# Optimization experiments

Hardware: AMD Instinct MI355X
Metric: run time of the kernel (lower is better)

Reference implementation:

```python
import jax, jax.numpy as jnp
import numpy as np

N_U, N_F = 50000, 20000
N = N_U + N_F
U_DIM, F_DIM, HID = 64, 128, 128
E = 2_000_000        # graph edges
E_PRED = 2_000_000   # prediction pairs
EPS = 1e-5
SLOPE = 0.01         # default leaky_relu negative slope


def setup_inputs() -> dict:
    key = jax.random.key(0)
    ks = jax.random.split(key, 20)
    s = 0.02
    inp = {
        "u_feat": jax.random.normal(ks[0], (N_U, U_DIM), jnp.float32),
        "f_feat": jax.random.normal(ks[1], (N_F, F_DIM), jnp.float32),
        "edge_index": jax.random.randint(ks[2], (2, E), 0, N, jnp.int64),
        "edge_u": jax.random.randint(ks[3], (E_PRED,), 0, N_U, jnp.int64),
        "edge_f": N_U + jax.random.randint(ks[4], (E_PRED,), 0, N_F, jnp.int64),
        # learned params
        "u_W": jax.random.normal(ks[5], (U_DIM, HID), jnp.float32) * s,
        "u_b": jnp.zeros((HID,), jnp.float32),
        "f_W": jax.random.normal(ks[6], (F_DIM, HID), jnp.float32) * s,
        "f_b": jnp.zeros((HID,), jnp.float32),
        "c1_W": jax.random.normal(ks[7], (HID, HID), jnp.float32) * s,
        "c1_b": jnp.zeros((HID,), jnp.float32),
        "c2_W": jax.random.normal(ks[8], (HID, HID), jnp.float32) * s,
        "c2_b": jnp.zeros((HID,), jnp.float32),
        "n1_g": jnp.ones((HID,), jnp.float32),
        "n1_b": jnp.zeros((HID,), jnp.float32),
        "n2_g": jnp.ones((HID,), jnp.float32),
        "n2_b": jnp.zeros((HID,), jnp.float32),
        "e_W": jax.random.normal(ks[9], (2 * HID, 1), jnp.float32) * s,
        "e_b": jnp.zeros((1,), jnp.float32),
        "r_W": jax.random.normal(ks[10], (2 * HID, 1), jnp.float32) * s,
        "r_b": jnp.zeros((1,), jnp.float32),
    }
    return inp


def _layer_norm(x, g, b):
    mu = jnp.mean(x, -1, keepdims=True)
    var = jnp.mean(jnp.square(x - mu), -1, keepdims=True)
    return (x - mu) * jax.lax.rsqrt(var + EPS) * g + b


def _gcn_conv(x, W, b, src, dst, n):
    # PyG GCNConv: add self loops, symmetric deg^{-1/2} norm, aggregate at dst.
    loop = jnp.arange(n, dtype=src.dtype)
    src_f = jnp.concatenate([src, loop])
    dst_f = jnp.concatenate([dst, loop])
    deg = jax.ops.segment_sum(jnp.ones(src_f.shape, x.dtype), dst_f, num_segments=n)
    dinv = jnp.where(deg > 0, jax.lax.rsqrt(deg), 0.0)
    norm = dinv[src_f] * dinv[dst_f]                     # [E+N]
    xw = x @ W                                           # [N, H]
    agg = jax.ops.segment_sum(xw[src_f] * norm[:, None], dst_f, num_segments=n)
    return agg + b


def reference(u_feat, f_feat, edge_index, edge_u, edge_f,
              u_W, u_b, f_W, f_b, c1_W, c1_b, c2_W, c2_b,
              n1_g, n1_b, n2_g, n2_b, e_W, e_b, r_W, r_b):
    src, dst = edge_index[0], edge_index[1]
    x = jnp.concatenate([u_feat @ u_W + u_b, f_feat @ f_W + f_b], 0)  # [N, H]
    x = jax.nn.leaky_relu(_layer_norm(_gcn_conv(x, c1_W, c1_b, src, dst, N), n1_g, n1_b), SLOPE)
    # dropout is identity in eval mode
    x = jax.nn.leaky_relu(_layer_norm(_gcn_conv(x, c2_W, c2_b, src, dst, N), n2_g, n2_b), SLOPE)
    emb = jnp.concatenate([x[edge_u], x[edge_f]], -1)                 # [E_pred, 2H]
    exist = jax.nn.sigmoid((emb @ e_W + e_b)[..., 0])
    rating = 1.0 + 4.0 * jax.nn.sigmoid((emb @ r_W + r_b)[..., 0])
    return exist, rating
```

## Files before the change

### kernel.cpp

```cpp
#include <hip/hip_runtime.h>
#include <hip/hip_bf16.h>
#include <math.h>

#define HID 128
#define SLOPE 0.01f
#define LN_EPS 1e-5f
#define NB_SCAN 256
#define NT_SCAN 256
#define BSHIFT 6
#define CHUNK 8192
#define MAXBUCK 1152

typedef __attribute__((ext_vector_type(8))) short bf16x8;
typedef __attribute__((ext_vector_type(4))) float f32x4;

__device__ __forceinline__ float bf16lo(unsigned int v) {
  unsigned int b = v << 16;
  return __builtin_bit_cast(float, b);
}
__device__ __forceinline__ float bf16hi(unsigned int v) {
  unsigned int b = v & 0xFFFF0000u;
  return __builtin_bit_cast(float, b);
}
__device__ __forceinline__ unsigned int pack_bf16(float lo, float hi) {
  __hip_bfloat16 a = __float2bfloat16(lo);
  __hip_bfloat16 b = __float2bfloat16(hi);
  return (unsigned int)__builtin_bit_cast(unsigned short, a) |
         ((unsigned int)__builtin_bit_cast(unsigned short, b) << 16);
}

__global__ __launch_bounds__(256) void wt_prep_kernel(
    const float* __restrict__ u_W, const float* __restrict__ f_W,
    const float* __restrict__ c1_W, const float* __restrict__ c2_W,
    const float* __restrict__ u_b, const float* __restrict__ f_b,
    unsigned int* __restrict__ wt_u1, unsigned int* __restrict__ wt_f1,
    unsigned int* __restrict__ wt_c2, float* __restrict__ bc_u,
    float* __restrict__ bc_f) {
  int idx = blockIdx.x * 256 + threadIdx.x;
  if (idx < 4096) {
    int col = idx & 127, k2 = idx >> 7;
    const float* a0 = u_W + (size_t)(2 * k2) * 128;
    const float* a1 = a0 + 128;
    float s0 = 0.0f, s1 = 0.0f;
    for (int m = 0; m < 128; ++m) {
      float bm = c1_W[(size_t)m * 128 + col];
      s0 = fmaf(a0[m], bm, s0);
      s1 = fmaf(a1[m], bm, s1);
    }
    wt_u1[(size_t)col * 32 + k2] = pack_bf16(s0, s1);
  } else if (idx < 12288) {
    int i = idx - 4096;
    int col = i & 127, k2 = i >> 7;
    const float* a0 = f_W + (size_t)(2 * k2) * 128;
    const float* a1 = a0 + 128;
    float s0 = 0.0f, s1 = 0.0f;
    for (int m = 0; m < 128; ++m) {
      float bm = c1_W[(size_t)m * 128 + col];
      s0 = fmaf(a0[m], bm, s0);
      s1 = fmaf(a1[m], bm, s1);
    }
    wt_f1[(size_t)col * 64 + k2] = pack_bf16(s0, s1);
  } else if (idx < 20480) {
    int i = idx - 12288;
    int col = i & 127, k2 = i >> 7;
    wt_c2[(size_t)col * 64 + k2] =
        pack_bf16(c2_W[(size_t)(2 * k2) * 128 + col],
                  c2_W[(size_t)(2 * k2 + 1) * 128 + col]);
  } else if (idx < 20736) {
    int i = idx - 20480;
    int j = i & 127;
    const float* bv = (i < 128) ? u_b : f_b;
    float s = 0.0f;
    for (int m = 0; m < 128; ++m) s = fmaf(bv[m], c1_W[(size_t)m * 128 + j], s);
    if (i < 128) bc_u[j] = s; else bc_f[j] = s;
  }
}

__global__ __launch_bounds__(256) void hist_chunk_kernel(
    const int* __restrict__ dst, int* __restrict__ cntM,
    int E, int nbuck, int nchunk) {
  __shared__ int hist[MAXBUCK];
  int c = blockIdx.x, tid = threadIdx.x;
  for (int i = tid; i < nbuck; i += 256) hist[i] = 0;
  __syncthreads();
  int beg = c * CHUNK, end = min(beg + CHUNK, E);
  for (int e = beg + tid; e < end; e += 256)
    atomicAdd(&hist[dst[e] >> BSHIFT], 1);
  __syncthreads();
  for (int b = tid; b < nbuck; b += 256)
    cntM[(size_t)b * nchunk + c] = hist[b];
}

__global__ void scan_pass1(const int* __restrict__ cnt, int* __restrict__ blocksum, int m) {
  __shared__ int ss[NT_SCAN];
  int K = (m + NB_SCAN * NT_SCAN - 1) / (NB_SCAN * NT_SCAN);
  int t = threadIdx.x, b = blockIdx.x;
  int beg = (b * NT_SCAN + t) * K;
  int end = min(beg + K, m);
  int s = 0;
  for (int i = beg; i < end; ++i) s += cnt[i];
  ss[t] = s;
  __syncthreads();
  for (int off = NT_SCAN / 2; off > 0; off >>= 1) {
    if (t < off) ss[t] += ss[t + off];
    __syncthreads();
  }
  if (t == 0) blocksum[b] = ss[0];
}

__global__ void scan_pass2(int* __restrict__ blocksum) {
  __shared__ int ss[NB_SCAN];
  int t = threadIdx.x;
  ss[t] = blocksum[t];
  __syncthreads();
  for (int off = 1; off < NB_SCAN; off <<= 1) {
    int v = (t >= off) ? ss[t - off] : 0;
    __syncthreads();
    ss[t] += v;
    __syncthreads();
  }
  blocksum[t] = (t == 0) ? 0 : ss[t - 1];
}

__global__ void scan_pass3(const int* __restrict__ cnt, const int* __restrict__ blockoff,
                           int* __restrict__ scanM, int m) {
  __shared__ int ss[NT_SCAN];
  int K = (m + NB_SCAN * NT_SCAN - 1) / (NB_SCAN * NT_SCAN);
  int t = threadIdx.x, b = blockIdx.x;
  int beg = (b * NT_SCAN + t) * K;
  int end = min(beg + K, m);
  int s = 0;
  for (int i = beg; i < end; ++i) s += cnt[i];
  ss[t] = s;
  __syncthreads();
  for (int off = 1; off < NT_SCAN; off <<= 1) {
    int v = (t >= off) ? ss[t - off] : 0;
    __syncthreads();
    ss[t] += v;
    __syncthreads();
  }
  int pre = blockoff[b] + ((t == 0) ? 0 : ss[t - 1]);
  for (int i = beg; i < end; ++i) {
    scanM[i] = pre;
    pre += cnt[i];
    if (i == m - 1) scanM[m] = pre;
  }
}

__global__ __launch_bounds__(256) void scatter_chunk_kernel(
    const int* __restrict__ src, const int* __restrict__ dst,
    const int* __restrict__ scanM, unsigned int* __restrict__ ebuf,
    int E, int nbuck, int nchunk) {
  __shared__ int cur[MAXBUCK];
  int c = blockIdx.x, tid = threadIdx.x;
  for (int b = tid; b < nbuck; b += 256)
    cur[b] = scanM[(size_t)b * nchunk + c];
  __syncthreads();
  int beg = c * CHUNK, end = min(beg + CHUNK, E);
  for (int e = beg + tid; e < end; e += 256) {
    int s = src[e], d = dst[e];
    int pos = atomicAdd(&cur[d >> BSHIFT], 1);
    ebuf[pos] = ((unsigned)s << 6) | ((unsigned)d & 63);
  }
}

__global__ __launch_bounds__(256) void deg_rowptr_kernel(
    const unsigned int* __restrict__ ebuf, const int* __restrict__ scanM,
    int* __restrict__ rowptr, float* __restrict__ dinv,
    int n, int nbuck, int nchunk, int E) {
  __shared__ int sdeg[64];
  int b = blockIdx.x, tid = threadIdx.x;
  if (tid < 64) sdeg[tid] = 0;
  __syncthreads();
  int beg = scanM[(size_t)b * nchunk], end = scanM[(size_t)(b + 1) * nchunk];
  for (int j = beg + tid; j < end; j += 256) atomicAdd(&sdeg[ebuf[j] & 63], 1);
  __syncthreads();
  if (tid < 64) {
    int deg = sdeg[tid];
    int s = deg;
#pragma unroll
    for (int off = 1; off < 64; off <<= 1) {
      int v = __shfl_up(s, off);
      if (tid >= off) s += v;
    }
    int excl = s - deg;
    int nd = (b << BSHIFT) + tid;
    if (nd < n) {
      rowptr[nd] = beg + excl;
      dinv[nd] = rsqrtf((float)(deg + 1));
    }
    if (b == nbuck - 1 && tid == 0) rowptr[n] = E;
  }
}

__global__ __launch_bounds__(256) void fill_bucket_kernel(
    const unsigned int* __restrict__ ebuf, const int* __restrict__ scanM,
    const int* __restrict__ rowptr, const float* __restrict__ dinv,
    uint2* __restrict__ ecol, int n, int nchunk) {
  __shared__ int scur[64];
  __shared__ int srow[64];
  __shared__ float sdinv[64];
  int b = blockIdx.x, tid = threadIdx.x;
  if (tid < 64) {
    scur[tid] = 0;
    int nd = (b << BSHIFT) + tid;
    srow[tid] = (nd < n) ? rowptr[nd] : 0;
    sdinv[tid] = (nd < n) ? dinv[nd] : 0.0f;
  }
  __syncthreads();
  int beg = scanM[(size_t)b * nchunk], end = scanM[(size_t)(b + 1) * nchunk];
  for (int j = beg + tid; j < end; j += 256) {
    unsigned int v = ebuf[j];
    int ndl = (int)(v & 63);
    int s = (int)(v >> 6);
    int pos = atomicAdd(&scur[ndl], 1);
    float w = dinv[s] * sdinv[ndl];
    ecol[srow[ndl] + pos] = make_uint2((unsigned)s, __builtin_bit_cast(unsigned int, w));
  }
}

template<int K, bool BF16OUT>
__global__ __launch_bounds__(256) void dense_mfma_kernel(
    const float* __restrict__ feat, const unsigned int* __restrict__ Wt,
    const float* __restrict__ bias,
    float* __restrict__ outf, __hip_bfloat16* __restrict__ outb, int nrows) {
  int tid = threadIdx.x;
  int wid = tid >> 6, lane = tid & 63;
  int l15 = lane & 15, lk = lane >> 4;
  int rowbase = blockIdx.x * 32 + 16 * (wid & 1);
  int colbase = 64 * (wid >> 1);

  f32x4 acc0 = {}, acc1 = {}, acc2 = {}, acc3 = {};

  int row = rowbase + l15;
  int rrow = min(row, nrows - 1);
  const float* ap0 = feat + (size_t)rrow * K + lk * 8;

#pragma unroll
  for (int kb = 0; kb < K / 32; ++kb) {
    const float* ap = ap0 + kb * 32;
    float4 a0 = *reinterpret_cast<const float4*>(ap);
    float4 a1 = *reinterpret_cast<const float4*>(ap + 4);
    float af0 = a0.x, af1 = a0.y, af2 = a0.z, af3 = a0.w;
    float af4 = a1.x, af5 = a1.y, af6 = a1.z, af7 = a1.w;
    unsigned int b0 = __builtin_bit_cast(unsigned int, af0);
    unsigned int b1 = __builtin_bit_cast(unsigned int, af1);
    unsigned int b2 = __builtin_bit_cast(unsigned int, af2);
    unsigned int b3 = __builtin_bit_cast(unsigned int, af3);
    unsigned int b4 = __builtin_bit_cast(unsigned int, af4);
    unsigned int b5 = __builtin_bit_cast(unsigned int, af5);
    unsigned int b6 = __builtin_bit_cast(unsigned int, af6);
    unsigned int b7 = __builtin_bit_cast(unsigned int, af7);
    uint4 hv;
    hv.x = (b0 >> 16) | (b1 & 0xFFFF0000u);
    hv.y = (b2 >> 16) | (b3 & 0xFFFF0000u);
    hv.z = (b4 >> 16) | (b5 & 0xFFFF0000u);
    hv.w = (b6 >> 16) | (b7 & 0xFFFF0000u);
    uint4 lv;
    {
      float h0 = __builtin_bit_cast(float, b0 & 0xFFFF0000u);
      float h1 = __builtin_bit_cast(float, b1 & 0xFFFF0000u);
      float h2 = __builtin_bit_cast(float, b2 & 0xFFFF0000u);
      float h3 = __builtin_bit_cast(float, b3 & 0xFFFF0000u);
      float h4 = __builtin_bit_cast(float, b4 & 0xFFFF0000u);
      float h5 = __builtin_bit_cast(float, b5 & 0xFFFF0000u);
      float h6 = __builtin_bit_cast(float, b6 & 0xFFFF0000u);
      float h7 = __builtin_bit_cast(float, b7 & 0xFFFF0000u);
      lv.x = pack_bf16(af0 - h0, af1 - h1);
      lv.y = pack_bf16(af2 - h2, af3 - h3);
      lv.z = pack_bf16(af4 - h4, af5 - h5);
      lv.w = pack_bf16(af6 - h6, af7 - h7);
    }
    bf16x8 ahi = __builtin_bit_cast(bf16x8, hv);
    bf16x8 alo = __builtin_bit_cast(bf16x8, lv);

    const unsigned int* wrow = Wt + (size_t)(colbase + l15) * (K / 2) + kb * 16 + lk * 4;
    bf16x8 bf0 = __builtin_bit_cast(bf16x8, *reinterpret_cast<const uint4*>(wrow));
    bf16x8 bf1 = __builtin_bit_cast(bf16x8, *reinterpret_cast<const uint4*>(wrow + 16 * (K / 2)));
    bf16x8 bf2 = __builtin_bit_cast(bf16x8, *reinterpret_cast<const uint4*>(wrow + 32 * (K / 2)));
    bf16x8 bf3 = __builtin_bit_cast(bf16x8, *reinterpret_cast<const uint4*>(wrow + 48 * (K / 2)));
    acc0 = __builtin_amdgcn_mfma_f32_16x16x32_bf16(ahi, bf0, acc0, 0, 0, 0);
    acc0 = __builtin_amdgcn_mfma_f32_16x16x32_bf16(alo, bf0, acc0, 0, 0, 0);
    acc1 = __builtin_amdgcn_mfma_f32_16x16x32_bf16(ahi, bf1, acc1, 0, 0, 0);
    acc1 = __builtin_amdgcn_mfma_f32_16x16x32_bf16(alo, bf1, acc1, 0, 0, 0);
    acc2 = __builtin_amdgcn_mfma_f32_16x16x32_bf16(ahi, bf2, acc2, 0, 0, 0);
    acc2 = __builtin_amdgcn_mfma_f32_16x16x32_bf16(alo, bf2, acc2, 0, 0, 0);
    acc3 = __builtin_amdgcn_mfma_f32_16x16x32_bf16(ahi, bf3, acc3, 0, 0, 0);
    acc3 = __builtin_amdgcn_mfma_f32_16x16x32_bf16(alo, bf3, acc3, 0, 0, 0);
  }

#pragma unroll
  for (int t = 0; t < 4; ++t) {
    int col = colbase + 16 * t + l15;
    float bv = bias ? bias[col] : 0.0f;
    f32x4 a = (t == 0) ? acc0 : (t == 1) ? acc1 : (t == 2) ? acc2 : acc3;
#pragma unroll
    for (int r = 0; r < 4; ++r) {
      int orow = rowbase + lk * 4 + r;
      if (orow < nrows) {
        float v = a[r] + bv;
        if (BF16OUT) outb[(size_t)orow * HID + col] = __float2bfloat16(v);
        else         outf[(size_t)orow * HID + col] = v;
      }
    }
  }
}

template<bool PROJ>
__global__ void gather_norm_kernel(const int* __restrict__ rowptr,
                                   const uint2* __restrict__ ecol,
                                   const uint4* __restrict__ xwb4,
                                   const float* __restrict__ dinv,
                                   const float* __restrict__ cb,
                                   const float* __restrict__ g,
                                   const float* __restrict__ b,
                                   const float* __restrict__ eW,
                                   const float* __restrict__ rW,
                                   float* __restrict__ outx,
                                   float4* __restrict__ table, int n_nodes) {
  int d = blockIdx.x * 4 + (threadIdx.x >> 6);
  if (d >= n_nodes) return;
  int lane = threadIdx.x & 63;
  int grp = lane >> 4;
  int t = lane & 15;

  float acc[8];
#pragma unroll
  for (int k = 0; k < 8; ++k) acc[k] = 0.0f;

  float wd = dinv[d];
  int beg = rowptr[d], end = rowptr[d + 1];
  int j = beg + grp;
  for (; j + 12 < end; j += 16) {
    uint2 e0 = ecol[j];
    uint2 e1 = ecol[j + 4];
    uint2 e2 = ecol[j + 8];
    uint2 e3 = ecol[j + 12];
    uint4 v0 = xwb4[(size_t)e0.x * 16 + t];
    uint4 v1 = xwb4[(size_t)e1.x * 16 + t];
    uint4 v2 = xwb4[(size_t)e2.x * 16 + t];
    uint4 v3 = xwb4[(size_t)e3.x * 16 + t];
    float w0 = __builtin_bit_cast(float, e0.y);
    float w1 = __builtin_bit_cast(float, e1.y);
    float w2 = __builtin_bit_cast(float, e2.y);
    float w3 = __builtin_bit_cast(float, e3.y);
    acc[0] = fmaf(bf16lo(v0.x), w0, acc[0]);
    acc[1] = fmaf(bf16hi(v0.x), w0, acc[1]);
    acc[2] = fmaf(bf16lo(v0.y), w0, acc[2]);
    acc[3] = fmaf(bf16hi(v0.y), w0, acc[3]);
    acc[4] = fmaf(bf16lo(v0.z), w0, acc[4]);
    acc[5] = fmaf(bf16hi(v0.z), w0, acc[5]);
    acc[6] = fmaf(bf16lo(v0.w), w0, acc[6]);
    acc[7] = fmaf(bf16hi(v0.w), w0, acc[7]);
    acc[0] = fmaf(bf16lo(v1.x), w1, acc[0]);
    acc[1] = fmaf(bf16hi(v1.x), w1, acc[1]);
    acc[2] = fmaf(bf16lo(v1.y), w1, acc[2]);
    acc[3] = fmaf(bf16hi(v1.y), w1, acc[3]);
    acc[4] = fmaf(bf16lo(v1.z), w1, acc[4]);
    acc[5] = fmaf(bf16hi(v1.z), w1, acc[5]);
    acc[6] = fmaf(bf16lo(v1.w), w1, acc[6]);
    acc[7] = fmaf(bf16hi(v1.w), w1, acc[7]);
    acc[0] = fmaf(bf16lo(v2.x), w2, acc[0]);
    acc[1] = fmaf(bf16hi(v2.x), w2, acc[1]);
    acc[2] = fmaf(bf16lo(v2.y), w2, acc[2]);
    acc[3] = fmaf(bf16hi(v2.y), w2, acc[3]);
    acc[4] = fmaf(bf16lo(v2.z), w2, acc[4]);
    acc[5] = fmaf(bf16hi(v2.z), w2, acc[5]);
    acc[6] = fmaf(bf16lo(v2.w), w2, acc[6]);
    acc[7] = fmaf(bf16hi(v2.w), w2, acc[7]);
    acc[0] = fmaf(bf16lo(v3.x), w3, acc[0]);
    acc[1] = fmaf(bf16hi(v3.x), w3, acc[1]);
    acc[2] = fmaf(bf16lo(v3.y), w3, acc[2]);
    acc[3] = fmaf(bf16hi(v3.y), w3, acc[3]);
    acc[4] = fmaf(bf16lo(v3.z), w3, acc[4]);
    acc[5] = fmaf(bf16hi(v3.z), w3, acc[5]);
    acc[6] = fmaf(bf16lo(v3.w), w3, acc[6]);
    acc[7] = fmaf(bf16hi(v3.w), w3, acc[7]);
  }
  for (; j < end; j += 4) {
    uint2 e0 = ecol[j];
    uint4 v0 = xwb4[(size_t)e0.x * 16 + t];
    float w0 = __builtin_bit_cast(float, e0.y);
    acc[0] = fmaf(bf16lo(v0.x), w0, acc[0]);
    acc[1] = fmaf(bf16hi(v0.x), w0, acc[1]);
    acc[2] = fmaf(bf16lo(v0.y), w0, acc[2]);
    acc[3] = fmaf(bf16hi(v0.y), w0, acc[3]);
    acc[4] = fmaf(bf16lo(v0.z), w0, acc[4]);
    acc[5] = fmaf(bf16hi(v0.z), w0, acc[5]);
    acc[6] = fmaf(bf16lo(v0.w), w0, acc[6]);
    acc[7] = fmaf(bf16hi(v0.w), w0, acc[7]);
  }
#pragma unroll
  for (int k = 0; k < 8; ++k) {
    acc[k] += __shfl_xor(acc[k], 16);
    acc[k] += __shfl_xor(acc[k], 32);
  }
  {
    float wself = wd * wd;
    uint4 v = xwb4[(size_t)d * 16 + t];
    acc[0] = fmaf(bf16lo(v.x), wself, acc[0]);
    acc[1] = fmaf(bf16hi(v.x), wself, acc[1]);
    acc[2] = fmaf(bf16lo(v.y), wself, acc[2]);
    acc[3] = fmaf(bf16hi(v.y), wself, acc[3]);
    acc[4] = fmaf(bf16lo(v.z), wself, acc[4]);
    acc[5] = fmaf(bf16hi(v.z), wself, acc[5]);
    acc[6] = fmaf(bf16lo(v.w), wself, acc[6]);
    acc[7] = fmaf(bf16hi(v.w), wself, acc[7]);
    float4 c0 = *reinterpret_cast<const float4*>(cb + 8 * t);
    float4 c1 = *reinterpret_cast<const float4*>(cb + 8 * t + 4);
    acc[0] += c0.x; acc[1] += c0.y; acc[2] += c0.z; acc[3] += c0.w;
    acc[4] += c1.x; acc[5] += c1.y; acc[6] += c1.z; acc[7] += c1.w;
  }
  float s = acc[0] + acc[1] + acc[2] + acc[3] + acc[4] + acc[5] + acc[6] + acc[7];
#pragma unroll
  for (int m = 1; m < 16; m <<= 1) s += __shfl_xor(s, m);
  float mu = s * (1.0f / HID);
  float sq = 0.0f;
#pragma unroll
  for (int k = 0; k < 8; ++k) {
    acc[k] -= mu;
    sq = fmaf(acc[k], acc[k], sq);
  }
#pragma unroll
  for (int m = 1; m < 16; m <<= 1) sq += __shfl_xor(sq, m);
  float rs = rsqrtf(sq * (1.0f / HID) + LN_EPS);
  float4 g0 = *reinterpret_cast<const float4*>(g + 8 * t);
  float4 g1 = *reinterpret_cast<const float4*>(g + 8 * t + 4);
  float4 b0 = *reinterpret_cast<const float4*>(b + 8 * t);
  float4 b1 = *reinterpret_cast<const float4*>(b + 8 * t + 4);
  float o[8];
  o[0] = acc[0] * rs * g0.x + b0.x;
  o[1] = acc[1] * rs * g0.y + b0.y;
  o[2] = acc[2] * rs * g0.z + b0.z;
  o[3] = acc[3] * rs * g0.w + b0.w;
  o[4] = acc[4] * rs * g1.x + b1.x;
  o[5] = acc[5] * rs * g1.y + b1.y;
  o[6] = acc[6] * rs * g1.z + b1.z;
  o[7] = acc[7] * rs * g1.w + b1.w;
#pragma unroll
  for (int k = 0; k < 8; ++k) o[k] = o[k] >= 0.0f ? o[k] : SLOPE * o[k];

  if (!PROJ) {
    if (grp == 0) {
      float4* op = reinterpret_cast<float4*>(outx + (size_t)d * HID + 8 * t);
      op[0] = make_float4(o[0], o[1], o[2], o[3]);
      op[1] = make_float4(o[4], o[5], o[6], o[7]);
    }
  } else {
    float4 eu0 = *reinterpret_cast<const float4*>(eW + 8 * t);
    float4 eu1 = *reinterpret_cast<const float4*>(eW + 8 * t + 4);
    float4 ef0 = *reinterpret_cast<const float4*>(eW + HID + 8 * t);
    float4 ef1 = *reinterpret_cast<const float4*>(eW + HID + 8 * t + 4);
    float4 ru0 = *reinterpret_cast<const float4*>(rW + 8 * t);
    float4 ru1 = *reinterpret_cast<const float4*>(rW + 8 * t + 4);
    float4 rf0 = *reinterpret_cast<const float4*>(rW + HID + 8 * t);
    float4 rf1 = *reinterpret_cast<const float4*>(rW + HID + 8 * t + 4);
    float pa = o[0]*eu0.x + o[1]*eu0.y + o[2]*eu0.z + o[3]*eu0.w
             + o[4]*eu1.x + o[5]*eu1.y + o[6]*eu1.z + o[7]*eu1.w;
    float pb = o[0]*ef0.x + o[1]*ef0.y + o[2]*ef0.z + o[3]*ef0.w
             + o[4]*ef1.x + o[5]*ef1.y + o[6]*ef1.z + o[7]*ef1.w;
    float pc = o[0]*ru0.x + o[1]*ru0.y + o[2]*ru0.z + o[3]*ru0.w
             + o[4]*ru1.x + o[5]*ru1.y + o[6]*ru1.z + o[7]*ru1.w;
    float pd = o[0]*rf0.x + o[1]*rf0.y + o[2]*rf0.z + o[3]*rf0.w
             + o[4]*rf1.x + o[5]*rf1.y + o[6]*rf1.z + o[7]*rf1.w;
#pragma unroll
    for (int m = 1; m < 16; m <<= 1) {
      pa += __shfl_xor(pa, m);
      pb += __shfl_xor(pb, m);
      pc += __shfl_xor(pc, m);
      pd += __shfl_xor(pd, m);
    }
    if (lane == 0) table[d] = make_float4(pa, pb, pc, pd);
  }
}

__global__ void pair_kernel(const int* __restrict__ eu, const int* __restrict__ ef,
                            const float4* __restrict__ table,
                            const float* __restrict__ eb, const float* __restrict__ rb,
                            float* __restrict__ out_exist, float* __restrict__ out_rating,
                            int Ep) {
  int i = blockIdx.x * blockDim.x + threadIdx.x;
  if (i >= Ep) return;
  float4 tu = table[eu[i]];
  float4 tf = table[ef[i]];
  float pe = tu.x + tf.y + eb[0];
  float pr = tu.z + tf.w + rb[0];
  out_exist[i]  = 1.0f / (1.0f + expf(-pe));
  out_rating[i] = 1.0f + 4.0f / (1.0f + expf(-pr));
}

extern "C" void kernel_launch(void* const* d_in, const int* in_sizes, int n_in,
                              void* d_out, int out_size, void* d_ws, size_t ws_size,
                              hipStream_t stream) {
  const float* u_feat = (const float*)d_in[0];
  const float* f_feat = (const float*)d_in[1];
  const int*   ei     = (const int*)d_in[2];
  const int*   eu     = (const int*)d_in[3];
  const int*   ef     = (const int*)d_in[4];
  const float* u_W  = (const float*)d_in[5];
  const float* u_b  = (const float*)d_in[6];
  const float* f_W  = (const float*)d_in[7];
  const float* f_b  = (const float*)d_in[8];
  const float* c1_W = (const float*)d_in[9];
  const float* c1_b = (const float*)d_in[10];
  const float* c2_W = (const float*)d_in[11];
  const float* c2_b = (const float*)d_in[12];
  const float* n1_g = (const float*)d_in[13];
  const float* n1_b = (const float*)d_in[14];
  const float* n2_g = (const float*)d_in[15];
  const float* n2_b = (const float*)d_in[16];
  const float* e_W  = (const float*)d_in[17];
  const float* e_b  = (const float*)d_in[18];
  const float* r_W  = (const float*)d_in[19];
  const float* r_b  = (const float*)d_in[20];

  int n_u = in_sizes[0] / 64;
  int n_f = in_sizes[1] / HID;
  int n   = n_u + n_f;
  int E   = in_sizes[2] / 2;
  int Ep  = in_sizes[3];
  int nbuck  = (n + (1 << BSHIFT) - 1) >> BSHIFT;
  int nchunk = (E + CHUNK - 1) / CHUNK;
  int m      = nbuck * nchunk;

  const int* src = ei;
  const int* dst = ei + E;

  float*        x      = (float*)d_ws;
  unsigned int* xwb    = (unsigned int*)(x + (size_t)n * HID);
  float4*       table  = (float4*)(xwb + (size_t)n * (HID / 2));
  unsigned int* ebuf   = (unsigned int*)(table + n);
  uint2*        ecol   = (uint2*)(ebuf + E);
  float*        dinv   = (float*)(ecol + E);
  int*          rowptr = (int*)(dinv + n);
  int*          cntM   = rowptr + n + 1;
  int*          scanM  = cntM + m;
  int*          blocksum = scanM + m + 1;
  unsigned int* wt_u1  = (unsigned int*)(blocksum + NB_SCAN);
  unsigned int* wt_f1  = wt_u1 + 128 * 32;
  unsigned int* wt_c2  = wt_f1 + 128 * 64;
  float*        bc_u   = (float*)(wt_c2 + 128 * 64);
  float*        bc_f   = bc_u + 128;

  wt_prep_kernel<<<81, 256, 0, stream>>>(u_W, f_W, c1_W, c2_W, u_b, f_b,
                                         wt_u1, wt_f1, wt_c2, bc_u, bc_f);

  hist_chunk_kernel<<<nchunk, 256, 0, stream>>>(dst, cntM, E, nbuck, nchunk);
  scan_pass1<<<NB_SCAN, NT_SCAN, 0, stream>>>(cntM, blocksum, m);
  scan_pass2<<<1, NB_SCAN, 0, stream>>>(blocksum);
  scan_pass3<<<NB_SCAN, NT_SCAN, 0, stream>>>(cntM, blocksum, scanM, m);
  scatter_chunk_kernel<<<nchunk, 256, 0, stream>>>(src, dst, scanM, ebuf, E, nbuck, nchunk);

  deg_rowptr_kernel<<<nbuck, 256, 0, stream>>>(ebuf, scanM, rowptr, dinv,
                                               n, nbuck, nchunk, E);
  fill_bucket_kernel<<<nbuck, 256, 0, stream>>>(ebuf, scanM, rowptr, dinv, ecol,
                                                n, nchunk);

  dense_mfma_kernel<64, true><<<(n_u + 31) / 32, 256, 0, stream>>>(
      u_feat, wt_u1, bc_u, nullptr, (__hip_bfloat16*)xwb, n_u);
  dense_mfma_kernel<128, true><<<(n_f + 31) / 32, 256, 0, stream>>>(
      f_feat, wt_f1, bc_f, nullptr, ((__hip_bfloat16*)xwb) + (size_t)n_u * HID, n_f);
  gather_norm_kernel<false><<<(n + 3) / 4, 256, 0, stream>>>(
      rowptr, ecol, (const uint4*)xwb, dinv, c1_b, n1_g, n1_b,
      nullptr, nullptr, x, nullptr, n);

  dense_mfma_kernel<128, true><<<(n + 31) / 32, 256, 0, stream>>>(
      x, wt_c2, nullptr, nullptr, (__hip_bfloat16*)xwb, n);
  gather_norm_kernel<true><<<(n + 3) / 4, 256, 0, stream>>>(
      rowptr, ecol, (const uint4*)xwb, dinv, c2_b, n2_g, n2_b,
      e_W, r_W, nullptr, table, n);

  float* out_exist  = (float*)d_out;
  float* out_rating = out_exist + Ep;
  pair_kernel<<<(Ep + 255) / 256, 256, 0, stream>>>(eu, ef, table, e_b, r_b,
                                                    out_exist, out_rating, Ep);
}
```

Measured before the change: 305.4 us.

## Merge weight prep with histogram, fold scan pass2, vectorize edge loops

Folds the weight-prep kernel and the dst histogram into one launch using block-index dispatch. Scan pass2 is folded into pass3, with every block redundantly scanning the 256 block sums. The edge loops in scatter, degree and fill, plus the pair kernel, now handle two elements per thread with int2/uint2 loads. This removes two kernel launches and widens memory accesses. It relies on 8-byte alignment, which holds because the chunk and bucket bases are even only when the offsets are even; scanM offsets can be odd, so the uint2 loads from ebuf may be misaligned.

```diff
diff --git a/kernel.cpp b/kernel.cpp
--- a/kernel.cpp
+++ b/kernel.cpp
@@ -10,6 +10,7 @@
 #define BSHIFT 6
 #define CHUNK 8192
 #define MAXBUCK 1152
+#define WPREP_BLOCKS 81
 
 typedef __attribute__((ext_vector_type(8))) short bf16x8;
 typedef __attribute__((ext_vector_type(4))) float f32x4;
@@ -29,13 +30,33 @@
          ((unsigned int)__builtin_bit_cast(unsigned short, b) << 16);
 }
 
-__global__ __launch_bounds__(256) void wt_prep_kernel(
+__global__ __launch_bounds__(256) void prep_hist_kernel(
     const float* __restrict__ u_W, const float* __restrict__ f_W,
     const float* __restrict__ c1_W, const float* __restrict__ c2_W,
     const float* __restrict__ u_b, const float* __restrict__ f_b,
     unsigned int* __restrict__ wt_u1, unsigned int* __restrict__ wt_f1,
     unsigned int* __restrict__ wt_c2, float* __restrict__ bc_u,
-    float* __restrict__ bc_f) {
+    float* __restrict__ bc_f,
+    const int* __restrict__ dst, int* __restrict__ cntM,
+    int E, int nbuck, int nchunk) {
+  __shared__ int hist[MAXBUCK];
+  if (blockIdx.x >= WPREP_BLOCKS) {
+    int c = blockIdx.x - WPREP_BLOCKS, tid = threadIdx.x;
+    for (int i = tid; i < nbuck; i += 256) hist[i] = 0;
+    __syncthreads();
+    int beg = c * CHUNK, end = min(beg + CHUNK, E);
+    int e = beg + 2 * tid;
+    for (; e + 1 < end; e += 512) {
+      int2 d2 = *reinterpret_cast<const int2*>(&dst[e]);
+      atomicAdd(&hist[d2.x >> BSHIFT], 1);
+      atomicAdd(&hist[d2.y >> BSHIFT], 1);
+    }
+    if (e < end) atomicAdd(&hist[dst[e] >> BSHIFT], 1);
+    __syncthreads();
+    for (int b = tid; b < nbuck; b += 256)
+      cntM[(size_t)b * nchunk + c] = hist[b];
+    return;
+  }
   int idx = blockIdx.x * 256 + threadIdx.x;
   if (idx < 4096) {
     int col = idx & 127, k2 = idx >> 7;
@@ -76,21 +97,6 @@
   }
 }
 
-__global__ __launch_bounds__(256) void hist_chunk_kernel(
-    const int* __restrict__ dst, int* __restrict__ cntM,
-    int E, int nbuck, int nchunk) {
-  __shared__ int hist[MAXBUCK];
-  int c = blockIdx.x, tid = threadIdx.x;
-  for (int i = tid; i < nbuck; i += 256) hist[i] = 0;
-  __syncthreads();
-  int beg = c * CHUNK, end = min(beg + CHUNK, E);
-  for (int e = beg + tid; e < end; e += 256)
-    atomicAdd(&hist[dst[e] >> BSHIFT], 1);
-  __syncthreads();
-  for (int b = tid; b < nbuck; b += 256)
-    cntM[(size_t)b * nchunk + c] = hist[b];
-}
-
 __global__ void scan_pass1(const int* __restrict__ cnt, int* __restrict__ blocksum, int m) {
   __shared__ int ss[NT_SCAN];
   int K = (m + NB_SCAN * NT_SCAN - 1) / (NB_SCAN * NT_SCAN);
@@ -108,25 +114,21 @@
   if (t == 0) blocksum[b] = ss[0];
 }
 
-__global__ void scan_pass2(int* __restrict__ blocksum) {
-  __shared__ int ss[NB_SCAN];
-  int t = threadIdx.x;
-  ss[t] = blocksum[t];
+__global__ void scan_pass3(const int* __restrict__ cnt, const int* __restrict__ blocksum,
+                           int* __restrict__ scanM, int m) {
+  __shared__ int ss[NT_SCAN];
+  __shared__ int sb[NB_SCAN];
+  int K = (m + NB_SCAN * NT_SCAN - 1) / (NB_SCAN * NT_SCAN);
+  int t = threadIdx.x, b = blockIdx.x;
+  sb[t] = blocksum[t];
   __syncthreads();
   for (int off = 1; off < NB_SCAN; off <<= 1) {
-    int v = (t >= off) ? ss[t - off] : 0;
+    int v = (t >= off) ? sb[t - off] : 0;
     __syncthreads();
-    ss[t] += v;
+    sb[t] += v;
     __syncthreads();
   }
-  blocksum[t] = (t == 0) ? 0 : ss[t - 1];
-}
-
-__global__ void scan_pass3(const int* __restrict__ cnt, const int* __restrict__ blockoff,
-                           int* __restrict__ scanM, int m) {
-  __shared__ int ss[NT_SCAN];
-  int K = (m + NB_SCAN * NT_SCAN - 1) / (NB_SCAN * NT_SCAN);
-  int t = threadIdx.x, b = blockIdx.x;
+  int blockoff = (b == 0) ? 0 : sb[b - 1];
   int beg = (b * NT_SCAN + t) * K;
   int end = min(beg + K, m);
   int s = 0;
@@ -139,7 +141,7 @@
     ss[t] += v;
     __syncthreads();
   }
-  int pre = blockoff[b] + ((t == 0) ? 0 : ss[t - 1]);
+  int pre = blockoff + ((t == 0) ? 0 : ss[t - 1]);
   for (int i = beg; i < end; ++i) {
     scanM[i] = pre;
     pre += cnt[i];
@@ -157,7 +159,16 @@
     cur[b] = scanM[(size_t)b * nchunk + c];
   __syncthreads();
   int beg = c * CHUNK, end = min(beg + CHUNK, E);
-  for (int e = beg + tid; e < end; e += 256) {
+  int e = beg + 2 * tid;
+  for (; e + 1 < end; e += 512) {
+    int2 s2 = *reinterpret_cast<const int2*>(&src[e]);
+    int2 d2 = *reinterpret_cast<const int2*>(&dst[e]);
+    int p0 = atomicAdd(&cur[d2.x >> BSHIFT], 1);
+    ebuf[p0] = ((unsigned)s2.x << 6) | ((unsigned)d2.x & 63);
+    int p1 = atomicAdd(&cur[d2.y >> BSHIFT], 1);
+    ebuf[p1] = ((unsigned)s2.y << 6) | ((unsigned)d2.y & 63);
+  }
+  if (e < end) {
     int s = src[e], d = dst[e];
     int pos = atomicAdd(&cur[d >> BSHIFT], 1);
     ebuf[pos] = ((unsigned)s << 6) | ((unsigned)d & 63);
@@ -173,7 +184,13 @@
   if (tid < 64) sdeg[tid] = 0;
   __syncthreads();
   int beg = scanM[(size_t)b * nchunk], end = scanM[(size_t)(b + 1) * nchunk];
-  for (int j = beg + tid; j < end; j += 256) atomicAdd(&sdeg[ebuf[j] & 63], 1);
+  int j = beg + 2 * tid;
+  for (; j + 1 < end; j += 512) {
+    uint2 v2 = *reinterpret_cast<const uint2*>(&ebuf[j]);
+    atomicAdd(&sdeg[v2.x & 63], 1);
+    atomicAdd(&sdeg[v2.y & 63], 1);
+  }
+  if (j < end) atomicAdd(&sdeg[ebuf[j] & 63], 1);
   __syncthreads();
   if (tid < 64) {
     int deg = sdeg[tid];
@@ -209,7 +226,25 @@
   }
   __syncthreads();
   int beg = scanM[(size_t)b * nchunk], end = scanM[(size_t)(b + 1) * nchunk];
-  for (int j = beg + tid; j < end; j += 256) {
+  int j = beg + 2 * tid;
+  for (; j + 1 < end; j += 512) {
+    uint2 v2 = *reinterpret_cast<const uint2*>(&ebuf[j]);
+    {
+      int ndl = (int)(v2.x & 63);
+      int s = (int)(v2.x >> 6);
+      int pos = atomicAdd(&scur[ndl], 1);
+      float w = dinv[s] * sdinv[ndl];
+      ecol[srow[ndl] + pos] = make_uint2((unsigned)s, __builtin_bit_cast(unsigned int, w));
+    }
+    {
+      int ndl = (int)(v2.y & 63);
+      int s = (int)(v2.y >> 6);
+      int pos = atomicAdd(&scur[ndl], 1);
+      float w = dinv[s] * sdinv[ndl];
+      ecol[srow[ndl] + pos] = make_uint2((unsigned)s, __builtin_bit_cast(unsigned int, w));
+    }
+  }
+  if (j < end) {
     unsigned int v = ebuf[j];
     int ndl = (int)(v & 63);
     int s = (int)(v >> 6);
@@ -480,13 +515,29 @@
                             float* __restrict__ out_exist, float* __restrict__ out_rating,
                             int Ep) {
   int i = blockIdx.x * blockDim.x + threadIdx.x;
-  if (i >= Ep) return;
-  float4 tu = table[eu[i]];
-  float4 tf = table[ef[i]];
-  float pe = tu.x + tf.y + eb[0];
-  float pr = tu.z + tf.w + rb[0];
-  out_exist[i]  = 1.0f / (1.0f + expf(-pe));
-  out_rating[i] = 1.0f + 4.0f / (1.0f + expf(-pr));
+  int base = 2 * i;
+  if (base >= Ep) return;
+  float ebv = eb[0], rbv = rb[0];
+  if (base + 1 < Ep) {
+    int2 u2 = *reinterpret_cast<const int2*>(&eu[base]);
+    int2 f2 = *reinterpret_cast<const int2*>(&ef[base]);
+    float4 tu0 = table[u2.x];
+    float4 tf0 = table[f2.x];
+    float4 tu1 = table[u2.y];
+    float4 tf1 = table[f2.y];
+    float2 ex, ra;
+    ex.x = 1.0f / (1.0f + expf(-(tu0.x + tf0.y + ebv)));
+    ex.y = 1.0f / (1.0f + expf(-(tu1.x + tf1.y + ebv)));
+    ra.x = 1.0f + 4.0f / (1.0f + expf(-(tu0.z + tf0.w + rbv)));
+    ra.y = 1.0f + 4.0f / (1.0f + expf(-(tu1.z + tf1.w + rbv)));
+    *reinterpret_cast<float2*>(&out_exist[base]) = ex;
+    *reinterpret_cast<float2*>(&out_rating[base]) = ra;
+  } else {
+    float4 tu = table[eu[base]];
+    float4 tf = table[ef[base]];
+    out_exist[base]  = 1.0f / (1.0f + expf(-(tu.x + tf.y + ebv)));
+    out_rating[base] = 1.0f + 4.0f / (1.0f + expf(-(tu.z + tf.w + rbv)));
+  }
 }
 
 extern "C" void kernel_launch(void* const* d_in, const int* in_sizes, int n_in,
@@ -542,12 +593,11 @@
   float*        bc_u   = (float*)(wt_c2 + 128 * 64);
   float*        bc_f   = bc_u + 128;
 
-  wt_prep_kernel<<<81, 256, 0, stream>>>(u_W, f_W, c1_W, c2_W, u_b, f_b,
-                                         wt_u1, wt_f1, wt_c2, bc_u, bc_f);
-
-  hist_chunk_kernel<<<nchunk, 256, 0, stream>>>(dst, cntM, E, nbuck, nchunk);
+  prep_hist_kernel<<<WPREP_BLOCKS + nchunk, 256, 0, stream>>>(
+      u_W, f_W, c1_W, c2_W, u_b, f_b, wt_u1, wt_f1, wt_c2, bc_u, bc_f,
+      dst, cntM, E, nbuck, nchunk);
+
   scan_pass1<<<NB_SCAN, NT_SCAN, 0, stream>>>(cntM, blocksum, m);
-  scan_pass2<<<1, NB_SCAN, 0, stream>>>(blocksum);
   scan_pass3<<<NB_SCAN, NT_SCAN, 0, stream>>>(cntM, blocksum, scanM, m);
   scatter_chunk_kernel<<<nchunk, 256, 0, stream>>>(src, dst, scanM, ebuf, E, nbuck, nchunk);
 
@@ -572,6 +622,6 @@
 
   float* out_exist  = (float*)d_out;
   float* out_rating = out_exist + Ep;
-  pair_kernel<<<(Ep + 255) / 256, 256, 0, stream>>>(eu, ef, table, e_b, r_b,
-                                                    out_exist, out_rating, Ep);
-}
+  pair_kernel<<<((Ep + 1) / 2 + 255) / 256, 256, 0, stream>>>(
+      eu, ef, table, e_b, r_b, out_exist, out_rating, Ep);
+}
```

After: 294.0 us. 1.04x faster.
